# Optimization experiments

Measured on AMD Instinct MI355X. Metric: run time of the kernel, lower is better.

Reference implementation:

```python
import jax, jax.numpy as jnp
import numpy as np

N_NODES = 50000
N_EDGES = 800000
NF = 128
HC = 128
NC = 40


def sage_conv(x, src, dst, Wl, Wr, b, num_nodes):
    """PyG SAGEConv with mean aggregation:
    out = lin_l(mean_{j in N(i)} x_j) + lin_r(x_i), bias folded into lin_l."""
    msgs = x[src]                                             # [E, F] gather
    agg = jax.ops.segment_sum(msgs, dst, num_segments=num_nodes)  # [N, F]
    cnt = jax.ops.segment_sum(jnp.ones((src.shape[0],), dtype=x.dtype), dst,
                              num_segments=num_nodes)          # [N]
    mean = agg / jnp.clip(cnt, 1.0)[:, None]                   # mean aggregation
    return mean @ Wl.T + x @ Wr.T + b


def setup_inputs() -> dict:
    key = jax.random.key(0)
    k = jax.random.split(key, 8)
    x = jax.random.normal(k[0], (N_NODES, NF), dtype=jnp.float32)
    edge_index = jax.random.randint(k[1], (2, N_EDGES), 0, N_NODES, dtype=jnp.int32)
    s1 = 1.0 / np.sqrt(NF)
    s2 = 1.0 / np.sqrt(HC)
    Wl1 = jax.random.uniform(k[2], (HC, NF), jnp.float32, -s1, s1)
    Wr1 = jax.random.uniform(k[3], (HC, NF), jnp.float32, -s1, s1)
    b1 = jnp.zeros((HC,), jnp.float32)
    Wl2 = jax.random.uniform(k[4], (NC, HC), jnp.float32, -s2, s2)
    Wr2 = jax.random.uniform(k[5], (NC, HC), jnp.float32, -s2, s2)
    b2 = jnp.zeros((NC,), jnp.float32)
    return {"x": x, "edge_index": edge_index, "Wl1": Wl1, "Wr1": Wr1,
            "b1": b1, "Wl2": Wl2, "Wr2": Wr2, "b2": b2}


def reference(x, edge_index, Wl1, Wr1, b1, Wl2, Wr2, b2):
    src, dst = edge_index[0], edge_index[1]
    num_nodes = x.shape[0]
    emb = sage_conv(x, src, dst, Wl1, Wr1, b1, num_nodes)      # embedding_output
    h = jax.nn.relu(emb)
    # F.dropout with training=False is the identity (inference reference)
    logits = sage_conv(h, src, dst, Wl2, Wr2, b2, num_nodes)
    return (logits, emb)
```

## Files before the change

### kernel.cpp

```cpp
#include <hip/hip_runtime.h>
#include <hip/hip_bf16.h>
#include <stdint.h>

#define NODES 50000
#define EDGES 800000
#define CAP   64

typedef __attribute__((ext_vector_type(8))) short bf16x8;
typedef __attribute__((ext_vector_type(8))) unsigned short u16x8;
typedef __attribute__((ext_vector_type(4))) unsigned short u16x4;
typedef __attribute__((ext_vector_type(4))) float f32x4;
typedef unsigned short ushort_t;

__device__ __forceinline__ ushort_t f2bf(float f) {
    unsigned u = __float_as_uint(f);
    unsigned r = (u + 0x7fff + ((u >> 16) & 1)) >> 16;
    return (ushort_t)r;
}
__device__ __forceinline__ float bf2f(ushort_t h) {
    return __uint_as_float(((unsigned)h) << 16);
}

__global__ __launch_bounds__(256) void prep(
    const float* __restrict__ x, const int* __restrict__ src,
    const int* __restrict__ dst,
    const float* __restrict__ Wr1, const float* __restrict__ Wl1,
    const float* __restrict__ Wr2, const float* __restrict__ Wl2,
    int* __restrict__ deg, ushort_t* __restrict__ esrc,
    ushort_t* __restrict__ xbf, ushort_t* __restrict__ w1p,
    ushort_t* __restrict__ w2p) {
    int b = blockIdx.x;
    if (b < 3128) {
        int g = b & 7, chunk = b >> 3;
        int lo = g * 6250;
#pragma unroll
        for (int k = 0; k < 8; ++k) {
            int e = chunk * 2048 + k * 256 + threadIdx.x;
            if (e < EDGES) {
                int d = __builtin_nontemporal_load(dst + e);
                if ((unsigned)(d - lo) < 6250u) {
                    int s = __builtin_nontemporal_load(src + e);
                    int p = atomicAdd(&deg[d], 1);
                    if (p < CAP) esrc[(size_t)d * CAP + p] = (ushort_t)s;
                }
            }
        }
    } else if (b < 9378) {
        int idx = (b - 3128) * 256 + threadIdx.x;
        int i = idx >> 5, c = idx & 31;
        f32x4 v = __builtin_nontemporal_load(
            reinterpret_cast<const f32x4*>(x + (size_t)i * 128 + c * 4));
        u16x4 h;
        h[0] = f2bf(v[0]); h[1] = f2bf(v[1]); h[2] = f2bf(v[2]); h[3] = f2bf(v[3]);
        *reinterpret_cast<u16x4*>(xbf + (size_t)i * 128 + c * 4) = h;
    } else if (b < 9394) {
        int t = (b - 9378) * 256 + threadIdx.x;
        int nf = t >> 9, kc = (t >> 6) & 7, lane = t & 63;
        int r = nf * 16 + (lane & 15);
        int k2 = kc * 32 + ((lane >> 4) << 3);
        u16x8 o;
#pragma unroll
        for (int j = 0; j < 8; ++j) {
            int kk = k2 + j;
            float v = (kk < 128) ? Wr1[r * 128 + kk] : Wl1[r * 128 + (kk - 128)];
            o[j] = f2bf(v);
        }
        *reinterpret_cast<u16x8*>(w1p + (size_t)t * 8) = o;
    } else {
        int t = (b - 9394) * 256 + threadIdx.x;
        if (t >= 1280) return;
        int nf = t >> 8, kc = (t >> 6) & 3, lane = t & 63;
        int r = nf * 16 + (lane & 15);
        int k2 = kc * 32 + ((lane >> 4) << 3);
        u16x8 o;
#pragma unroll
        for (int j = 0; j < 8; ++j) {
            int kk = k2 + j;
            float v = (r < 40) ? Wr2[r * 128 + kk] : Wl2[(r - 40) * 128 + kk];
            o[j] = f2bf(v);
        }
        *reinterpret_cast<u16x8*>(w2p + (size_t)t * 8) = o;
    }
}

__global__ __launch_bounds__(256) void aggx(
    const ushort_t* __restrict__ xbf, ushort_t* __restrict__ mbf,
    const ushort_t* __restrict__ esrc, const int* __restrict__ deg) {
    int idx = blockIdx.x * 256 + threadIdx.x;
    int i = idx >> 4, c = idx & 15;
    if (i >= NODES) return;
    int dg = deg[i];
    int n = dg < CAP ? dg : CAP;
    const ushort_t* ep = esrc + (size_t)i * CAP;
    float a0[8] = {}, a1[8] = {};
    int j = 0;
    for (; j + 4 <= n; j += 4) {
        int s0 = ep[j], s1 = ep[j + 1], s2 = ep[j + 2], s3 = ep[j + 3];
        u16x8 v0 = *reinterpret_cast<const u16x8*>(xbf + (size_t)s0 * 128 + c * 8);
        u16x8 v1 = *reinterpret_cast<const u16x8*>(xbf + (size_t)s1 * 128 + c * 8);
        u16x8 v2 = *reinterpret_cast<const u16x8*>(xbf + (size_t)s2 * 128 + c * 8);
        u16x8 v3 = *reinterpret_cast<const u16x8*>(xbf + (size_t)s3 * 128 + c * 8);
#pragma unroll
        for (int k = 0; k < 8; ++k) {
            a0[k] += bf2f(v0[k]) + bf2f(v2[k]);
            a1[k] += bf2f(v1[k]) + bf2f(v3[k]);
        }
    }
    for (; j < n; ++j) {
        int s = ep[j];
        u16x8 v = *reinterpret_cast<const u16x8*>(xbf + (size_t)s * 128 + c * 8);
#pragma unroll
        for (int k = 0; k < 8; ++k) a0[k] += bf2f(v[k]);
    }
    float ci = 1.0f / fmaxf((float)dg, 1.0f);
    u16x8 m;
#pragma unroll
    for (int k = 0; k < 8; ++k) m[k] = f2bf((a0[k] + a1[k]) * ci);
    *reinterpret_cast<u16x8*>(mbf + (size_t)i * 128 + c * 8) = m;
}

__global__ __launch_bounds__(256) void gemm12(
    const ushort_t* __restrict__ xbf, const ushort_t* __restrict__ mbf,
    const ushort_t* __restrict__ w1p, const ushort_t* __restrict__ w2p,
    const float* __restrict__ b1, float* __restrict__ emb,
    ushort_t* __restrict__ V, int M) {
    __shared__ ushort_t hs[64][136];
    const int wave = threadIdx.x >> 6, lane = threadIdx.x & 63;
    const int r0 = blockIdx.x * 64 + wave * 16;
    int arow = r0 + (lane & 15); if (arow >= M) arow = M - 1;
    const int klane = (lane >> 4) * 8;

    f32x4 acc[8] = {};
#pragma unroll
    for (int kc = 0; kc < 8; ++kc) {
        const ushort_t* abase = (kc < 4) ? xbf : mbf;
        bf16x8 a = *reinterpret_cast<const bf16x8*>(
            abase + (size_t)arow * 128 + (kc & 3) * 32 + klane);
        bf16x8 wv[8];
#pragma unroll
        for (int nf = 0; nf < 8; ++nf)
            wv[nf] = *reinterpret_cast<const bf16x8*>(
                w1p + (size_t)((nf * 8 + kc) * 64 + lane) * 8);
#pragma unroll
        for (int nf = 0; nf < 8; ++nf)
            acc[nf] = __builtin_amdgcn_mfma_f32_16x16x32_bf16(a, wv[nf], acc[nf], 0, 0, 0);
    }

    const int crow0r = wave * 16 + (lane >> 4) * 4;
    const int crow0  = blockIdx.x * 64 + crow0r;
    const int ccol   = lane & 15;
#pragma unroll
    for (int nf = 0; nf < 8; ++nf) {
        int col = nf * 16 + ccol;
        float bv = b1[col];
#pragma unroll
        for (int r = 0; r < 4; ++r) {
            int row = crow0 + r;
            float val = acc[nf][r] + bv;
            if (row < M)
                __builtin_nontemporal_store(val, emb + (size_t)row * 128 + col);
            hs[crow0r + r][col] = f2bf(fmaxf(val, 0.f));
        }
    }
    __syncthreads();

    f32x4 acc2[5] = {};
#pragma unroll
    for (int kc = 0; kc < 4; ++kc) {
        bf16x8 a = *reinterpret_cast<const bf16x8*>(
            &hs[wave * 16 + (lane & 15)][kc * 32 + klane]);
        bf16x8 wv[5];
#pragma unroll
        for (int nf = 0; nf < 5; ++nf)
            wv[nf] = *reinterpret_cast<const bf16x8*>(
                w2p + (size_t)((nf * 4 + kc) * 64 + lane) * 8);
#pragma unroll
        for (int nf = 0; nf < 5; ++nf)
            acc2[nf] = __builtin_amdgcn_mfma_f32_16x16x32_bf16(a, wv[nf], acc2[nf], 0, 0, 0);
    }
#pragma unroll
    for (int nf = 0; nf < 5; ++nf) {
        int col = nf * 16 + ccol;
#pragma unroll
        for (int r = 0; r < 4; ++r) {
            int row = crow0 + r;
            if (row < M) V[(size_t)row * 80 + col] = f2bf(acc2[nf][r]);
        }
    }
}

__global__ __launch_bounds__(256) void agg2(
    const ushort_t* __restrict__ V, const ushort_t* __restrict__ esrc,
    const int* __restrict__ deg, const float* __restrict__ b2,
    float* __restrict__ logits) {
    int idx = blockIdx.x * 256 + threadIdx.x;
    int i = idx >> 3, c = idx & 7;
    if (i >= NODES || c >= 5) return;
    int dg = deg[i];
    int n = dg < CAP ? dg : CAP;
    const ushort_t* ep = esrc + (size_t)i * CAP;
    float a0[8] = {}, a1[8] = {};
    int j = 0;
    for (; j + 4 <= n; j += 4) {
        int s0 = ep[j], s1 = ep[j + 1], s2 = ep[j + 2], s3 = ep[j + 3];
        u16x8 v0 = *reinterpret_cast<const u16x8*>(V + (size_t)s0 * 80 + 40 + c * 8);
        u16x8 v1 = *reinterpret_cast<const u16x8*>(V + (size_t)s1 * 80 + 40 + c * 8);
        u16x8 v2 = *reinterpret_cast<const u16x8*>(V + (size_t)s2 * 80 + 40 + c * 8);
        u16x8 v3 = *reinterpret_cast<const u16x8*>(V + (size_t)s3 * 80 + 40 + c * 8);
#pragma unroll
        for (int k = 0; k < 8; ++k) {
            a0[k] += bf2f(v0[k]) + bf2f(v2[k]);
            a1[k] += bf2f(v1[k]) + bf2f(v3[k]);
        }
    }
    for (; j < n; ++j) {
        int s = ep[j];
        u16x8 v = *reinterpret_cast<const u16x8*>(V + (size_t)s * 80 + 40 + c * 8);
#pragma unroll
        for (int k = 0; k < 8; ++k) a0[k] += bf2f(v[k]);
    }
    float ci = 1.0f / fmaxf((float)dg, 1.0f);
    u16x8 sv = *reinterpret_cast<const u16x8*>(V + (size_t)i * 80 + c * 8);
    float o[8];
#pragma unroll
    for (int k = 0; k < 8; ++k)
        o[k] = bf2f(sv[k]) + (a0[k] + a1[k]) * ci + b2[c * 8 + k];
    float4* dst4 = reinterpret_cast<float4*>(logits + (size_t)i * 40 + c * 8);
    dst4[0] = make_float4(o[0], o[1], o[2], o[3]);
    dst4[1] = make_float4(o[4], o[5], o[6], o[7]);
}

extern "C" void kernel_launch(void* const* d_in, const int* in_sizes, int n_in,
                              void* d_out, int out_size, void* d_ws, size_t ws_size,
                              hipStream_t stream) {
    const float* x   = (const float*)d_in[0];
    const int*   ei  = (const int*)d_in[1];
    const float* Wl1 = (const float*)d_in[2];
    const float* Wr1 = (const float*)d_in[3];
    const float* b1  = (const float*)d_in[4];
    const float* Wl2 = (const float*)d_in[5];
    const float* Wr2 = (const float*)d_in[6];
    const float* b2  = (const float*)d_in[7];
    const int* src = ei;
    const int* dst = ei + EDGES;

    char* ws = (char*)d_ws;
    ushort_t* xbf  = (ushort_t*)ws;
    ushort_t* mbf  = (ushort_t*)(ws + 12800000);
    ushort_t* V    = (ushort_t*)(ws + 25600000);
    ushort_t* esrc = (ushort_t*)(ws + 33600000);
    int*      deg  = (int*)(ws + 40000000);
    ushort_t* w1p  = (ushort_t*)(ws + 40200000);
    ushort_t* w2p  = (ushort_t*)(ws + 40265536);

    float* logits_out = (float*)d_out;
    float* emb_out    = logits_out + (size_t)NODES * 40;

    hipMemsetAsync(deg, 0, (size_t)NODES * 4, stream);

    prep<<<9399, 256, 0, stream>>>(x, src, dst, Wr1, Wl1, Wr2, Wl2,
                                   deg, esrc, xbf, w1p, w2p);

    aggx<<<3125, 256, 0, stream>>>(xbf, mbf, esrc, deg);

    gemm12<<<(NODES + 63) / 64, 256, 0, stream>>>(xbf, mbf, w1p, w2p, b1,
                                                  emb_out, V, NODES);

    agg2<<<(NODES * 8 + 255) / 256, 256, 0, stream>>>(V, esrc, deg, b2, logits_out);
}
```

Baseline: 126.2 us.

## Bucket edges by destination group before building per-node adjacency lists

```diff
diff --git a/kernel.cpp b/kernel.cpp
--- a/kernel.cpp
+++ b/kernel.cpp
@@ -5,6 +5,8 @@
 #define NODES 50000
 #define EDGES 800000
 #define CAP   64
+#define GRP   6250
+#define BINCAP 131072
 
 typedef __attribute__((ext_vector_type(8))) short bf16x8;
 typedef __attribute__((ext_vector_type(8))) unsigned short u16x8;
@@ -21,40 +23,58 @@
     return __uint_as_float(((unsigned)h) << 16);
 }
 
-__global__ __launch_bounds__(256) void prep(
+__global__ __launch_bounds__(256) void prepA(
     const float* __restrict__ x, const int* __restrict__ src,
     const int* __restrict__ dst,
     const float* __restrict__ Wr1, const float* __restrict__ Wl1,
     const float* __restrict__ Wr2, const float* __restrict__ Wl2,
-    int* __restrict__ deg, ushort_t* __restrict__ esrc,
+    unsigned* __restrict__ bins, unsigned* __restrict__ bin_cnt,
     ushort_t* __restrict__ xbf, ushort_t* __restrict__ w1p,
     ushort_t* __restrict__ w2p) {
     int b = blockIdx.x;
-    if (b < 3128) {
-        int g = b & 7, chunk = b >> 3;
-        int lo = g * 6250;
-#pragma unroll
-        for (int k = 0; k < 8; ++k) {
-            int e = chunk * 2048 + k * 256 + threadIdx.x;
-            if (e < EDGES) {
-                int d = __builtin_nontemporal_load(dst + e);
-                if ((unsigned)(d - lo) < 6250u) {
-                    int s = __builtin_nontemporal_load(src + e);
-                    int p = atomicAdd(&deg[d], 1);
-                    if (p < CAP) esrc[(size_t)d * CAP + p] = (ushort_t)s;
+    if (b < 391) {
+        __shared__ int lcnt[8];
+        __shared__ unsigned lbase[8];
+        __shared__ unsigned lbin[8][1024];
+        int t = threadIdx.x;
+        for (int tile = 0; tile < 2; ++tile) {
+            if (t < 8) lcnt[t] = 0;
+            __syncthreads();
+            int e0 = (b * 2 + tile) * 1024;
+#pragma unroll
+            for (int k = 0; k < 4; ++k) {
+                int e = e0 + k * 256 + t;
+                if (e < EDGES) {
+                    int d = dst[e], s = src[e];
+                    int g = d / GRP;
+                    int slot = atomicAdd(&lcnt[g], 1);
+                    lbin[g][slot] = ((unsigned)(d - g * GRP) << 16) | (unsigned)s;
                 }
             }
-        }
-    } else if (b < 9378) {
-        int idx = (b - 3128) * 256 + threadIdx.x;
+            __syncthreads();
+            if (t < 8) lbase[t] = atomicAdd(&bin_cnt[t], (unsigned)lcnt[t]);
+            __syncthreads();
+            for (int g = 0; g < 8; ++g) {
+                int cnt = lcnt[g];
+                unsigned base = lbase[g];
+                for (int i = t; i < cnt; i += 256) {
+                    unsigned idx = base + i;
+                    if (idx < BINCAP)
+                        bins[(size_t)g * BINCAP + idx] = lbin[g][i];
+                }
+            }
+            __syncthreads();
+        }
+    } else if (b < 6641) {
+        int idx = (b - 391) * 256 + threadIdx.x;
         int i = idx >> 5, c = idx & 31;
         f32x4 v = __builtin_nontemporal_load(
             reinterpret_cast<const f32x4*>(x + (size_t)i * 128 + c * 4));
         u16x4 h;
         h[0] = f2bf(v[0]); h[1] = f2bf(v[1]); h[2] = f2bf(v[2]); h[3] = f2bf(v[3]);
         *reinterpret_cast<u16x4*>(xbf + (size_t)i * 128 + c * 4) = h;
-    } else if (b < 9394) {
-        int t = (b - 9378) * 256 + threadIdx.x;
+    } else if (b < 6657) {
+        int t = (b - 6641) * 256 + threadIdx.x;
         int nf = t >> 9, kc = (t >> 6) & 7, lane = t & 63;
         int r = nf * 16 + (lane & 15);
         int k2 = kc * 32 + ((lane >> 4) << 3);
@@ -67,7 +87,7 @@
         }
         *reinterpret_cast<u16x8*>(w1p + (size_t)t * 8) = o;
     } else {
-        int t = (b - 9394) * 256 + threadIdx.x;
+        int t = (b - 6657) * 256 + threadIdx.x;
         if (t >= 1280) return;
         int nf = t >> 8, kc = (t >> 6) & 3, lane = t & 63;
         int r = nf * 16 + (lane & 15);
@@ -80,6 +100,23 @@
             o[j] = f2bf(v);
         }
         *reinterpret_cast<u16x8*>(w2p + (size_t)t * 8) = o;
+    }
+}
+
+__global__ __launch_bounds__(256) void prepB(
+    const unsigned* __restrict__ bins, const unsigned* __restrict__ bin_cnt,
+    int* __restrict__ deg, ushort_t* __restrict__ esrc) {
+    int g = blockIdx.x & 7, chunk = blockIdx.x >> 3;
+    unsigned cnt = bin_cnt[g];
+    if (cnt > BINCAP) cnt = BINCAP;
+    const unsigned* bp = bins + (size_t)g * BINCAP;
+    int base = g * GRP;
+    for (unsigned i = chunk * 256 + threadIdx.x; i < cnt; i += 49 * 256) {
+        unsigned pk = bp[i];
+        int d = base + (int)(pk >> 16);
+        int s = (int)(pk & 0xffffu);
+        int p = atomicAdd(&deg[d], 1);
+        if (p < CAP) esrc[(size_t)d * CAP + p] = (ushort_t)s;
     }
 }
 
@@ -245,21 +282,25 @@
     const int* dst = ei + EDGES;
 
     char* ws = (char*)d_ws;
-    ushort_t* xbf  = (ushort_t*)ws;
-    ushort_t* mbf  = (ushort_t*)(ws + 12800000);
-    ushort_t* V    = (ushort_t*)(ws + 25600000);
-    ushort_t* esrc = (ushort_t*)(ws + 33600000);
-    int*      deg  = (int*)(ws + 40000000);
-    ushort_t* w1p  = (ushort_t*)(ws + 40200000);
-    ushort_t* w2p  = (ushort_t*)(ws + 40265536);
+    ushort_t* xbf     = (ushort_t*)ws;
+    ushort_t* mbf     = (ushort_t*)(ws + 12800000);
+    ushort_t* V       = (ushort_t*)(ws + 25600000);
+    ushort_t* esrc    = (ushort_t*)(ws + 33600000);
+    int*      deg     = (int*)(ws + 40000000);
+    unsigned* bin_cnt = (unsigned*)(ws + 40200000);
+    ushort_t* w1p     = (ushort_t*)(ws + 40200064);
+    ushort_t* w2p     = (ushort_t*)(ws + 40265600);
+    unsigned* bins    = (unsigned*)(ws + 40286080);
 
     float* logits_out = (float*)d_out;
     float* emb_out    = logits_out + (size_t)NODES * 40;
 
-    hipMemsetAsync(deg, 0, (size_t)NODES * 4, stream);
-
-    prep<<<9399, 256, 0, stream>>>(x, src, dst, Wr1, Wl1, Wr2, Wl2,
-                                   deg, esrc, xbf, w1p, w2p);
+    hipMemsetAsync(deg, 0, 200064, stream);
+
+    prepA<<<6662, 256, 0, stream>>>(x, src, dst, Wr1, Wl1, Wr2, Wl2,
+                                    bins, bin_cnt, xbf, w1p, w2p);
+
+    prepB<<<392, 256, 0, stream>>>(bins, bin_cnt, deg, esrc);
 
     aggx<<<3125, 256, 0, stream>>>(xbf, mbf, esrc, deg);
 
```

After: 133.4 us. 1.06x slower.
